# Kernel tuning notes

Measured on AMD Instinct MI355X. Metric: run time of the kernel, lower is better.

Reference implementation:

```python
import jax, jax.numpy as jnp
import numpy as np
import math

D_MODEL = 1024
N_HEADS = 16
D_HEAD = D_MODEL // N_HEADS
DECAY_MAX = 0.99  # buggy torch init: only the LAST head's decay rate survives the loop
LN_EPS = 1e-5


def setup_inputs() -> dict:
    key = jax.random.key(0)
    ks = jax.random.split(key, 12)
    B, S = 2, 2048
    x = jax.random.normal(ks[0], (B, S, D_MODEL), dtype=jnp.float32)
    def w(k):
        return jax.random.normal(k, (D_MODEL, D_MODEL), dtype=jnp.float32) * 0.02
    return {
        "x": x,
        "Wq": w(ks[1]), "bq": jnp.zeros((D_MODEL,), jnp.float32),
        "Wk": w(ks[2]), "bk": jnp.zeros((D_MODEL,), jnp.float32),
        "Wv": w(ks[3]), "bv": jnp.zeros((D_MODEL,), jnp.float32),
        "Wg": w(ks[4]), "bg": jnp.zeros((D_MODEL,), jnp.float32),
        "Wo": w(ks[5]), "bo": jnp.zeros((D_MODEL,), jnp.float32),
        "gamma": jnp.ones((D_MODEL,), jnp.float32),
        "beta": jnp.zeros((D_MODEL,), jnp.float32),
    }


def _decay_mask(S):
    # faithful to torch buffer: decay_matrix[i,j] = DECAY_MAX**(i-j) for j<=i else 0
    i = jnp.arange(S, dtype=jnp.float32)[:, None]
    j = jnp.arange(S, dtype=jnp.float32)[None, :]
    diff = i - j
    return jnp.where(diff >= 0, jnp.power(jnp.float32(DECAY_MAX), diff), 0.0)  # [S,S]


def reference(x, Wq, bq, Wk, bk, Wv, bv, Wg, bg, Wo, bo, gamma, beta):
    B, S, D = x.shape
    H, DH = N_HEADS, D_HEAD
    # projections -> [B,H,S,DH]
    Q = (x @ Wq + bq).reshape(B, S, H, DH).transpose(0, 2, 1, 3)
    K = (x @ Wk + bk).reshape(B, S, H, DH).transpose(0, 2, 1, 3)
    V = (x @ Wv + bv).reshape(B, S, H, DH).transpose(0, 2, 1, 3)
    scores = jnp.einsum('bhsd,bhtd->bhst', Q, K) / math.sqrt(DH)  # [B,H,S,S]
    mask = _decay_mask(S)  # [S,S], broadcast over B,H (head-independent per torch bug)
    retained = jnp.einsum('bhst,bhtd->bhsd', scores * mask, V)
    retained = retained.transpose(0, 2, 1, 3).reshape(B, S, D)
    # LayerNorm over last dim
    mu = jnp.mean(retained, axis=-1, keepdims=True)
    var = jnp.var(retained, axis=-1, keepdims=True)
    normed = (retained - mu) * jax.lax.rsqrt(var + LN_EPS) * gamma + beta
    G = jax.nn.sigmoid(x @ Wg + bg)
    return (normed * G) @ Wo + bo  # dropout = identity (eval)
```

## Files before the change

### kernel.cpp

```cpp
#include <hip/hip_runtime.h>

typedef __attribute__((ext_vector_type(4))) float f32x4;
typedef __attribute__((ext_vector_type(8))) short bf16x8;
typedef unsigned short USHORT;

static __device__ __forceinline__ float bf2f(USHORT u) {
    return __uint_as_float(((unsigned)u) << 16);
}
static __device__ __forceinline__ USHORT f2bf(float f) {
    unsigned u = __float_as_uint(f);
    unsigned r = u + 0x7FFF + ((u >> 16) & 1);
    return (USHORT)(r >> 16);
}

#define GLDS16(gp, lp) __builtin_amdgcn_global_load_lds(                      \
    (const __attribute__((address_space(1))) unsigned int*)(gp),              \
    (__attribute__((address_space(3))) unsigned int*)(lp), 16, 0, 0)

#define FULL_BARRIER() asm volatile("s_waitcnt vmcnt(0) lgkmcnt(0)\ns_barrier" ::: "memory")

#define D64 0.52559648f
#define L2D (-0.014499569695115089f)

struct PrepArgs { const float* src[5]; USHORT* dst[5]; const float* x; USHORT* xb; };

__global__ __launch_bounds__(256) void k_prep(PrepArgs pa) {
    const int z = blockIdx.z;
    const int tid = threadIdx.x;
    __shared__ USHORT t[64][65];
    if (z < 5) {
        const float* __restrict__ W  = pa.src[z];
        USHORT* __restrict__      WT = pa.dst[z];
        const int k0 = blockIdx.y * 64, n0 = blockIdx.x * 64;
#pragma unroll
        for (int s = 0; s < 4; s++) {
            int slot = tid + s * 256;
            int row = slot >> 4, c4 = (slot & 15) * 4;
            float4 vv = *(const float4*)&W[(size_t)(k0 + row) * 1024 + n0 + c4];
            t[row][c4 + 0] = f2bf(vv.x);
            t[row][c4 + 1] = f2bf(vv.y);
            t[row][c4 + 2] = f2bf(vv.z);
            t[row][c4 + 3] = f2bf(vv.w);
        }
        __syncthreads();
#pragma unroll
        for (int s = 0; s < 2; s++) {
            int slot = tid + s * 256;
            int n = slot >> 3, c8 = (slot & 7) * 8;
            USHORT tmp[8];
#pragma unroll
            for (int u = 0; u < 8; u++) tmp[u] = t[c8 + u][n];
            *(int4*)&WT[(size_t)(n0 + n) * 1024 + k0 + c8] = *(int4*)tmp;
        }
    } else {
        const int bi = blockIdx.y * 16 + blockIdx.x;
        const float* xs = pa.x + (size_t)bi * 16384;
        USHORT* xd = pa.xb + (size_t)bi * 16384;
#pragma unroll
        for (int u = 0; u < 16; u++) {
            int idx = u * 1024 + tid * 4;
            float4 v = *(const float4*)&xs[idx];
            *(ushort4*)&xd[idx] = make_ushort4(f2bf(v.x), f2bf(v.y), f2bf(v.z), f2bf(v.w));
        }
    }
}

struct GArgs {
    const USHORT* A;
    const USHORT* W[4];
    const float*  bias[4];
    void*         dst[4];
    USHORT*       dstv;
    float         scale[4];
    int           mode[4];
};

__global__ __launch_bounds__(256, 2) void k_gemm(GArgs ga) {
    const int z = blockIdx.z;
    const USHORT* __restrict__ A  = ga.A;
    const USHORT* __restrict__ BT = ga.W[z];
    __shared__ USHORT As[2][128 * 32];
    __shared__ USHORT Bs[2][128 * 32];
    const int tid = threadIdx.x;
    const int m0 = blockIdx.y * 128, n0 = blockIdx.x * 128;
    const int w = tid >> 6, l = tid & 63, lr = l & 15, q = l >> 4;
    const int wr = w >> 1, wc = w & 1;
    const int srow = tid >> 2, sco = (tid & 3) * 8;
    f32x4 acc[4][4] = {};
    GLDS16(&A [(size_t)(m0 + srow)      * 1024 + sco], &As[0][srow * 32 + sco]);
    GLDS16(&A [(size_t)(m0 + srow + 64) * 1024 + sco], &As[0][(srow + 64) * 32 + sco]);
    GLDS16(&BT[(size_t)(n0 + srow)      * 1024 + sco], &Bs[0][srow * 32 + sco]);
    GLDS16(&BT[(size_t)(n0 + srow + 64) * 1024 + sco], &Bs[0][(srow + 64) * 32 + sco]);
    for (int kt = 0; kt < 32; kt++) {
        const int cur = kt & 1;
        FULL_BARRIER();
        if (kt + 1 < 32) {
            const int k1 = (kt + 1) * 32;
            const int nxt = 1 - cur;
            GLDS16(&A [(size_t)(m0 + srow)      * 1024 + k1 + sco], &As[nxt][srow * 32 + sco]);
            GLDS16(&A [(size_t)(m0 + srow + 64) * 1024 + k1 + sco], &As[nxt][(srow + 64) * 32 + sco]);
            GLDS16(&BT[(size_t)(n0 + srow)      * 1024 + k1 + sco], &Bs[nxt][srow * 32 + sco]);
            GLDS16(&BT[(size_t)(n0 + srow + 64) * 1024 + k1 + sco], &Bs[nxt][(srow + 64) * 32 + sco]);
        }
        bf16x8 af[4], bfr[4];
#pragma unroll
        for (int mi = 0; mi < 4; mi++)
            af[mi] = *(const bf16x8*)&As[cur][(wr * 64 + mi * 16 + lr) * 32 + q * 8];
#pragma unroll
        for (int ni = 0; ni < 4; ni++)
            bfr[ni] = *(const bf16x8*)&Bs[cur][(wc * 64 + ni * 16 + lr) * 32 + q * 8];
#pragma unroll
        for (int mi = 0; mi < 4; mi++)
#pragma unroll
            for (int ni = 0; ni < 4; ni++)
                acc[mi][ni] = __builtin_amdgcn_mfma_f32_16x16x32_bf16(
                    af[mi], bfr[ni], acc[mi][ni], 0, 0, 0);
    }
    const float scale = ga.scale[z];
    const int mode = ga.mode[z];
    const float* __restrict__ bias = ga.bias[z];
#pragma unroll
    for (int ni = 0; ni < 4; ni++) {
        int col = n0 + wc * 64 + ni * 16 + lr;
        float bv = bias[col];
#pragma unroll
        for (int mi = 0; mi < 4; mi++) {
            int r0 = m0 + wr * 64 + mi * 16 + q * 4;
            float vr[4];
#pragma unroll
            for (int r = 0; r < 4; r++) {
                float v = acc[mi][ni][r] + bv;
                if (mode == 1) v = 1.0f / (1.0f + __expf(-v));
                vr[r] = v * scale;
            }
            if (mode == 3) {
                float* df = (float*)ga.dst[z];
#pragma unroll
                for (int r = 0; r < 4; r++)
                    df[(size_t)(r0 + r) * 1024 + col] = vr[r];
            } else if (mode == 2) {
                int b = r0 >> 11, s = r0 & 2047;
                int h = col >> 6, d = col & 63;
                const float NP1 = 1.0101010101010102f;
                float c0 = exp2f(-L2D * (float)(s & 63));
                float c1 = c0 * NP1, c2 = c1 * NP1, c3 = c2 * NP1;
                *(ushort4*)&ga.dstv[(size_t)(((b * 16 + h) * 64) + d) * 2048 + s] =
                    make_ushort4(f2bf(vr[0] * c0), f2bf(vr[1] * c1),
                                 f2bf(vr[2] * c2), f2bf(vr[3] * c3));
            } else {
                USHORT* db = (USHORT*)ga.dst[z];
#pragma unroll
                for (int r = 0; r < 4; r++)
                    db[(size_t)(r0 + r) * 1024 + col] = f2bf(vr[r]);
            }
        }
    }
}

__global__ __launch_bounds__(256) void k_attn_u(const USHORT* __restrict__ K,
                                                const USHORT* __restrict__ VT,
                                                float* __restrict__ U) {
    const int bh = blockIdx.x, c = blockIdx.y;
    const int b = bh >> 4, h = bh & 15;
    const int tid = threadIdx.x, w = tid >> 6, l = tid & 63, lr = l & 15, q = l >> 4;
    __shared__ USHORT KT[64 * 72];
    __shared__ USHORT Vs[64 * 72];
#pragma unroll
    for (int s = 0; s < 2; s++) {
        int slot = tid + s * 256;
        int row = slot >> 3, co = (slot & 7) * 8;
        USHORT kv[8];
        *(int4*)kv = *(const int4*)&K[(size_t)(b * 2048 + c * 64 + row) * 1024 + h * 64 + co];
#pragma unroll
        for (int u = 0; u < 8; u++) KT[(co + u) * 72 + row] = kv[u];
        *(int4*)&Vs[row * 72 + co] =
            *(const int4*)&VT[(size_t)(bh * 64 + row) * 2048 + c * 64 + co];
    }
    __syncthreads();
    f32x4 acc[4] = {};
    bf16x8 av[2];
#pragma unroll
    for (int kk = 0; kk < 2; kk++)
        av[kk] = *(const bf16x8*)&Vs[(w * 16 + lr) * 72 + kk * 32 + q * 8];
#pragma unroll
    for (int dkt = 0; dkt < 4; dkt++)
#pragma unroll
        for (int kk = 0; kk < 2; kk++) {
            bf16x8 bk = *(const bf16x8*)&KT[(dkt * 16 + lr) * 72 + kk * 32 + q * 8];
            acc[dkt] = __builtin_amdgcn_mfma_f32_16x16x32_bf16(av[kk], bk, acc[dkt], 0, 0, 0);
        }
    float* slot = U + (size_t)(bh * 32 + c) * 4096;
#pragma unroll
    for (int dkt = 0; dkt < 4; dkt++)
#pragma unroll
        for (int r = 0; r < 4; r++)
            slot[(w * 16 + q * 4 + r) * 64 + dkt * 16 + lr] = acc[dkt][r] * D64;
}

__global__ __launch_bounds__(256, 2) void k_apply(const USHORT* __restrict__ Q,
                                                  const USHORT* __restrict__ K,
                                                  const USHORT* __restrict__ VT,
                                                  const float* __restrict__ U,
                                                  USHORT* __restrict__ R,
                                                  float* __restrict__ stats) {
    const int bh = blockIdx.x, c = blockIdx.y;
    const int b = bh >> 4, h = bh & 15;
    const int i0 = c * 64;
    const int tid = threadIdx.x, w = tid >> 6, l = tid & 63, lr = l & 15, q = l >> 4;
    __shared__ USHORT Qs[64 * 72];
    __shared__ USHORT Ks[64 * 72];
    __shared__ USHORT Vs[64 * 72];
    __shared__ USHORT Ps[4][16 * 72];
    __shared__ unsigned Spk[4096];
#pragma unroll
    for (int s = 0; s < 2; s++) {
        int slot = tid + s * 256;
        int row = slot >> 3, c8 = (slot & 7) * 8;
        USHORT q8[8];
        *(int4*)q8 = *(const int4*)&Q[(size_t)(b * 2048 + i0 + row) * 1024 + h * 64 + c8];
        const float fr = exp2f(L2D * (float)row);
#pragma unroll
        for (int u = 0; u < 8; u++) q8[u] = f2bf(bf2f(q8[u]) * fr);
        *(int4*)&Qs[row * 72 + c8] = *(int4*)q8;
        *(int4*)&Ks[row * 72 + c8] =
            *(const int4*)&K[(size_t)(b * 2048 + i0 + row) * 1024 + h * 64 + c8];
        *(int4*)&Vs[row * 72 + c8] =
            *(const int4*)&VT[(size_t)(bh * 64 + row) * 2048 + i0 + c8];
    }
    if (c > 0) {
        float sa[16] = {};
        const float* Ub = U + (size_t)bh * 32 * 4096 + tid * 16;
        for (int cp = 0; cp < c; cp++) {
            const float* p = Ub + (size_t)cp * 4096;
#pragma unroll
            for (int u4 = 0; u4 < 4; u4++) {
                float4 uv = *(const float4*)(p + u4 * 4);
                sa[u4 * 4 + 0] = sa[u4 * 4 + 0] * D64 + uv.x;
                sa[u4 * 4 + 1] = sa[u4 * 4 + 1] * D64 + uv.y;
                sa[u4 * 4 + 2] = sa[u4 * 4 + 2] * D64 + uv.z;
                sa[u4 * 4 + 3] = sa[u4 * 4 + 3] * D64 + uv.w;
            }
        }
#pragma unroll
        for (int u = 0; u < 16; u++) {
            USHORT hi = f2bf(sa[u]);
            float  lo = sa[u] - bf2f(hi);
            Spk[tid * 16 + u] = (unsigned)hi | ((unsigned)f2bf(lo) << 16);
        }
    }
    __syncthreads();
    bf16x8 bqf[2];
#pragma unroll
    for (int kk = 0; kk < 2; kk++)
        bqf[kk] = *(const bf16x8*)&Qs[(w * 16 + lr) * 72 + kk * 32 + q * 8];
    f32x4 accr[4] = {};
    if (c > 0) {
#pragma unroll
        for (int dt = 0; dt < 4; dt++)
#pragma unroll
            for (int kk = 0; kk < 2; kk++) {
                const unsigned* sp = &Spk[(dt * 16 + lr) * 64 + kk * 32 + q * 8];
                uint4 pa = *(const uint4*)sp;
                uint4 pb = *(const uint4*)(sp + 4);
                unsigned pk[8] = { pa.x, pa.y, pa.z, pa.w, pb.x, pb.y, pb.z, pb.w };
                bf16x8 hi, lo;
#pragma unroll
                for (int u = 0; u < 8; u++) {
                    hi[u] = (short)(pk[u] & 0xffffu);
                    lo[u] = (short)(pk[u] >> 16);
                }
                accr[dt] = __builtin_amdgcn_mfma_f32_16x16x32_bf16(hi, bqf[kk], accr[dt], 0, 0, 0);
                accr[dt] = __builtin_amdgcn_mfma_f32_16x16x32_bf16(lo, bqf[kk], accr[dt], 0, 0, 0);
            }
    }
    {
        f32x4 accp[4] = {};
#pragma unroll
        for (int kk = 0; kk < 2; kk++)
#pragma unroll
            for (int jt = 0; jt < 4; jt++) {
                bf16x8 akf = *(const bf16x8*)&Ks[(jt * 16 + lr) * 72 + kk * 32 + q * 8];
                accp[jt] = __builtin_amdgcn_mfma_f32_16x16x32_bf16(akf, bqf[kk], accp[jt], 0, 0, 0);
            }
        const int ii = w * 16 + lr;
#pragma unroll
        for (int jt = 0; jt < 4; jt++) {
            const int jj = jt * 16 + q * 4;
            float v0 = (jj + 0 <= ii) ? accp[jt][0] : 0.0f;
            float v1 = (jj + 1 <= ii) ? accp[jt][1] : 0.0f;
            float v2 = (jj + 2 <= ii) ? accp[jt][2] : 0.0f;
            float v3 = (jj + 3 <= ii) ? accp[jt][3] : 0.0f;
            unsigned w0 = __builtin_amdgcn_perm(
                __float_as_uint(v1), __float_as_uint(v0), 0x07060302u);
            unsigned w1 = __builtin_amdgcn_perm(
                __float_as_uint(v3), __float_as_uint(v2), 0x07060302u);
            *(uint2*)&Ps[w][lr * 72 + jt * 16 + q * 4] = make_uint2(w0, w1);
        }
        asm volatile("s_waitcnt lgkmcnt(0)" ::: "memory");
#pragma unroll
        for (int kk = 0; kk < 2; kk++) {
            bf16x8 bpf = *(const bf16x8*)&Ps[w][lr * 72 + kk * 32 + q * 8];
#pragma unroll
            for (int dt = 0; dt < 4; dt++) {
                bf16x8 avf = *(const bf16x8*)&Vs[(dt * 16 + lr) * 72 + kk * 32 + q * 8];
                accr[dt] = __builtin_amdgcn_mfma_f32_16x16x32_bf16(avf, bpf, accr[dt], 0, 0, 0);
            }
        }
    }
    {
        float s1 = 0.f, s2 = 0.f;
#pragma unroll
        for (int dt = 0; dt < 4; dt++)
#pragma unroll
            for (int r = 0; r < 4; r++) {
                float v = accr[dt][r];
                s1 += v; s2 += v * v;
            }
        s1 += __shfl_down(s1, 32); s2 += __shfl_down(s2, 32);
        s1 += __shfl_down(s1, 16); s2 += __shfl_down(s2, 16);
        if (q == 0) {
            int row = b * 2048 + i0 + w * 16 + lr;
            *(float2*)&stats[((size_t)row * 16 + h) * 2] = make_float2(s1, s2);
        }
    }
    {
        const int i = i0 + w * 16 + lr;
#pragma unroll
        for (int dt = 0; dt < 4; dt++) {
            f32x4 a = accr[dt];
            *(ushort4*)&R[(size_t)(b * 2048 + i) * 1024 + h * 64 + dt * 16 + q * 4] =
                make_ushort4(f2bf(a[0]), f2bf(a[1]), f2bf(a[2]), f2bf(a[3]));
        }
    }
}

__global__ __launch_bounds__(256) void k_ln_gate(const USHORT* __restrict__ R,
                                                 const USHORT* __restrict__ G,
                                                 const float* __restrict__ stats,
                                                 const float* __restrict__ gamma,
                                                 const float* __restrict__ beta,
                                                 USHORT* __restrict__ NG) {
    const int row = blockIdx.x, tid = threadIdx.x;
    float s1 = 0.f, s2 = 0.f;
    const float* sp = &stats[(size_t)row * 32];
#pragma unroll
    for (int hh = 0; hh < 8; hh++) {
        float4 v = *(const float4*)(sp + hh * 4);
        s1 += v.x + v.z; s2 += v.y + v.w;
    }
    const float mu  = s1 * (1.0f / 1024.0f);
    const float var = s2 * (1.0f / 1024.0f) - mu * mu;
    const float inv = rsqrtf(fmaxf(var, 0.0f) + 1e-5f);
    ushort4 rv = *(const ushort4*)&R[(size_t)row * 1024 + tid * 4];
    ushort4 g4 = *(const ushort4*)&G[(size_t)row * 1024 + tid * 4];
    float4 gm = *(const float4*)&gamma[tid * 4];
    float4 bt = *(const float4*)&beta[tid * 4];
    float  vv[4]  = { bf2f(rv.x), bf2f(rv.y), bf2f(rv.z), bf2f(rv.w) };
    USHORT gg[4]  = { g4.x, g4.y, g4.z, g4.w };
    float  gmm[4] = { gm.x, gm.y, gm.z, gm.w };
    float  btt[4] = { bt.x, bt.y, bt.z, bt.w };
    USHORT o4[4];
#pragma unroll
    for (int u = 0; u < 4; u++) {
        float nv = (vv[u] - mu) * inv * gmm[u] + btt[u];
        o4[u] = f2bf(nv * bf2f(gg[u]));
    }
    *(ushort4*)&NG[(size_t)row * 1024 + tid * 4] = make_ushort4(o4[0], o4[1], o4[2], o4[3]);
}

extern "C" void kernel_launch(void* const* d_in, const int* in_sizes, int n_in,
                              void* d_out, int out_size, void* d_ws, size_t ws_size,
                              hipStream_t stream) {
    const float* x     = (const float*)d_in[0];
    const float* Wq    = (const float*)d_in[1];
    const float* bq    = (const float*)d_in[2];
    const float* Wk    = (const float*)d_in[3];
    const float* bk    = (const float*)d_in[4];
    const float* Wv    = (const float*)d_in[5];
    const float* bv    = (const float*)d_in[6];
    const float* Wg    = (const float*)d_in[7];
    const float* bg    = (const float*)d_in[8];
    const float* Wo    = (const float*)d_in[9];
    const float* bo    = (const float*)d_in[10];
    const float* gamma = (const float*)d_in[11];
    const float* beta  = (const float*)d_in[12];

    char* ws = (char*)d_ws;
    const size_t MB = 1 << 20;
    USHORT* WqT = (USHORT*)(ws + 0 * MB);
    USHORT* WkT = (USHORT*)(ws + 2 * MB);
    USHORT* WvT = (USHORT*)(ws + 4 * MB);
    USHORT* WgT = (USHORT*)(ws + 6 * MB);
    USHORT* WoT = (USHORT*)(ws + 8 * MB);
    USHORT* Qb  = (USHORT*)(ws + 10 * MB);
    USHORT* Kb  = (USHORT*)(ws + 18 * MB);
    USHORT* VTb = (USHORT*)(ws + 26 * MB);
    USHORT* Gb  = (USHORT*)(ws + 34 * MB);
    float*  Sts = (float*) (ws + 42 * MB);
    USHORT* NGb = Qb;
    USHORT* Xb  = (USHORT*)d_out;
    float*  Ust = (float*)d_out;

    {
        PrepArgs pa;
        pa.src[0] = Wq; pa.src[1] = Wk; pa.src[2] = Wv; pa.src[3] = Wg; pa.src[4] = Wo;
        pa.dst[0] = WqT; pa.dst[1] = WkT; pa.dst[2] = WvT; pa.dst[3] = WgT; pa.dst[4] = WoT;
        pa.x = x; pa.xb = Xb;
        k_prep<<<dim3(16, 16, 6), 256, 0, stream>>>(pa);
    }
    {
        GArgs ga;
        ga.A = Xb;
        ga.W[0] = WqT; ga.W[1] = WkT; ga.W[2] = WvT; ga.W[3] = WgT;
        ga.bias[0] = bq; ga.bias[1] = bk; ga.bias[2] = bv; ga.bias[3] = bg;
        ga.dst[0] = Qb; ga.dst[1] = Kb; ga.dst[2] = nullptr; ga.dst[3] = Gb;
        ga.dstv = VTb;
        ga.scale[0] = 0.125f; ga.scale[1] = 1.0f; ga.scale[2] = 1.0f; ga.scale[3] = 1.0f;
        ga.mode[0] = 0; ga.mode[1] = 0; ga.mode[2] = 2; ga.mode[3] = 1;
        k_gemm<<<dim3(8, 32, 4), 256, 0, stream>>>(ga);
    }
    k_attn_u<<<dim3(32, 32), 256, 0, stream>>>(Kb, VTb, Ust);
    k_apply<<<dim3(32, 32), 256, 0, stream>>>(Qb, Kb, VTb, Ust, Kb, Sts);
    k_ln_gate<<<4096, 256, 0, stream>>>(Kb, Gb, Sts, gamma, beta, NGb);
    {
        GArgs go;
        go.A = NGb;
        for (int i = 0; i < 4; i++) {
            go.W[i] = WoT; go.bias[i] = bo; go.dst[i] = d_out;
            go.scale[i] = 1.0f; go.mode[i] = 3;
        }
        go.dstv = nullptr;
        k_gemm<<<dim3(8, 32, 1), 256, 0, stream>>>(go);
    }
}
```

Before: 221.7 us.

## Add 256x256-tile 8-wave pipelined GEMM for fused QKVG projection

Adds a new projection GEMM kernel with 256x256 output tiles, 512 threads and 128KB of dynamic LDS. It uses direct global-to-LDS loads with an XOR swizzle, a double-buffered half-K pipeline, and raised wave priority around the MFMA bursts. Larger tiles raise arithmetic intensity and cut global traffic for the four fused projections. The cost is a grid of only 256 blocks, which may underfill the GPU, plus heavy register and LDS pressure. The old kernel stays as a fallback if the LDS attribute cannot be set.

```diff
diff --git a/kernel.cpp b/kernel.cpp
--- a/kernel.cpp
+++ b/kernel.cpp
@@ -157,6 +157,131 @@
     }
 }
 
+#define LDSA(buf, kh) (((buf) * 2 + (kh)) * 8192)
+#define LDSB(buf, kh) (32768 + ((buf) * 2 + (kh)) * 8192)
+#define BAR() asm volatile("s_barrier" ::: "memory")
+#define VM8() asm volatile("s_waitcnt vmcnt(8)" ::: "memory")
+
+#define STAGE_A(ks, kh, buf) do {                                             \
+    const USHORT* s_ = aBase + (ks) * 64 + (kh) * 32;                         \
+    GLDS16(s_,          &lds[LDSA(buf, kh) + ldsT]);                          \
+    GLDS16(s_ + 131072, &lds[LDSA(buf, kh) + 4096 + ldsT]); } while (0)
+
+#define STAGE_B(ks, kh, buf) do {                                             \
+    const USHORT* s_ = bBase + (ks) * 64 + (kh) * 32;                         \
+    GLDS16(s_,          &lds[LDSB(buf, kh) + ldsT]);                          \
+    GLDS16(s_ + 131072, &lds[LDSB(buf, kh) + 4096 + ldsT]); } while (0)
+
+#define PHASE256(buf, kh, mg, LOADB, STAGE_STMT, WAITSTMT) do {               \
+    _Pragma("unroll")                                                         \
+    for (int mi = 0; mi < 4; mi++)                                            \
+        af[mi] = *(const bf16x8*)&lds[LDSA(buf, kh) + aoff + ((mg) * 4 + mi) * 512]; \
+    if (LOADB) {                                                              \
+        _Pragma("unroll")                                                     \
+        for (int ni = 0; ni < 4; ni++)                                        \
+            bfrag[ni] = *(const bf16x8*)&lds[LDSB(buf, kh) + boff + ni * 512];\
+    }                                                                         \
+    STAGE_STMT;                                                               \
+    BAR();                                                                    \
+    __builtin_amdgcn_s_setprio(1);                                            \
+    _Pragma("unroll")                                                         \
+    for (int mi = 0; mi < 4; mi++)                                            \
+        _Pragma("unroll")                                                     \
+        for (int ni = 0; ni < 4; ni++)                                        \
+            acc[(mg) * 4 + mi][ni] = __builtin_amdgcn_mfma_f32_16x16x32_bf16( \
+                af[mi], bfrag[ni], acc[(mg) * 4 + mi][ni], 0, 0, 0);          \
+    __builtin_amdgcn_s_setprio(0);                                            \
+    WAITSTMT;                                                                 \
+    BAR();                                                                    \
+} while (0)
+
+__global__ __launch_bounds__(512, 2) void k_gemm256(GArgs ga) {
+    extern __shared__ USHORT lds[];
+    int bid = blockIdx.x + 4 * (blockIdx.y + 16 * blockIdx.z);
+    bid = (bid & 7) * 32 + (bid >> 3);
+    const int bz = bid >> 6;
+    const int by = (bid >> 2) & 15;
+    const int bx = bid & 3;
+    const int z = bz;
+    const USHORT* __restrict__ A  = ga.A;
+    const USHORT* __restrict__ BT = ga.W[z];
+    const int m0 = by * 256, n0 = bx * 256;
+    const int tid = threadIdx.x;
+    const int wid = tid >> 6, l = tid & 63, lr = l & 15, q = l >> 4;
+    const int wr = wid >> 2, wc = wid & 3;
+    const int srow = tid >> 2;
+    const int scol = (((tid & 3) ^ ((tid >> 2) & 3)) << 3);
+    const USHORT* aBase = A  + (size_t)(m0 + srow) * 1024 + scol;
+    const USHORT* bBase = BT + (size_t)(n0 + srow) * 1024 + scol;
+    const int ldsT = tid * 8;
+    const int kread = ((q ^ (lr & 3)) << 3);
+    const int aoff = (wr * 128 + lr) * 32 + kread;
+    const int boff = (wc * 64 + lr) * 32 + kread;
+    f32x4 acc[8][4] = {};
+    bf16x8 af[4], bfrag[4];
+
+    STAGE_A(0, 0, 0); STAGE_B(0, 0, 0);
+    STAGE_A(0, 1, 0); STAGE_B(0, 1, 0);
+    STAGE_A(1, 0, 1); STAGE_B(1, 0, 1);
+    VM8();
+    BAR();
+
+    for (int kt = 0; kt < 16; kt += 2) {
+        const int ks1 = kt + 1;
+        const int ks2 = (kt + 2 < 16) ? kt + 2 : 15;
+        const int ks3 = (kt + 2 < 16) ? kt + 2 : 15;
+        const int ks4 = (kt + 3 < 16) ? kt + 3 : 15;
+        PHASE256(0, 0, 0, 1, STAGE_A(ks1, 1, 1), (void)0);
+        PHASE256(0, 0, 1, 0, STAGE_B(ks1, 1, 1), VM8());
+        PHASE256(0, 1, 0, 1, STAGE_A(ks2, 0, 0), (void)0);
+        PHASE256(0, 1, 1, 0, STAGE_B(ks2, 0, 0), VM8());
+        PHASE256(1, 0, 0, 1, STAGE_A(ks3, 1, 0), (void)0);
+        PHASE256(1, 0, 1, 0, STAGE_B(ks3, 1, 0), VM8());
+        PHASE256(1, 1, 0, 1, STAGE_A(ks4, 0, 1), (void)0);
+        PHASE256(1, 1, 1, 0, STAGE_B(ks4, 0, 1), VM8());
+    }
+
+    const float scale = ga.scale[z];
+    const int mode = ga.mode[z];
+    const float* __restrict__ bias = ga.bias[z];
+#pragma unroll
+    for (int ni = 0; ni < 4; ni++) {
+        int col = n0 + wc * 64 + ni * 16 + lr;
+        float bv = bias[col];
+#pragma unroll
+        for (int mi = 0; mi < 8; mi++) {
+            int r0 = m0 + wr * 128 + mi * 16 + q * 4;
+            float vr[4];
+#pragma unroll
+            for (int r = 0; r < 4; r++) {
+                float v = acc[mi][ni][r] + bv;
+                if (mode == 1) v = 1.0f / (1.0f + __expf(-v));
+                vr[r] = v * scale;
+            }
+            if (mode == 3) {
+                float* df = (float*)ga.dst[z];
+#pragma unroll
+                for (int r = 0; r < 4; r++)
+                    df[(size_t)(r0 + r) * 1024 + col] = vr[r];
+            } else if (mode == 2) {
+                int b = r0 >> 11, s = r0 & 2047;
+                int h = col >> 6, d = col & 63;
+                const float NP1 = 1.0101010101010102f;
+                float c0 = exp2f(-L2D * (float)(s & 63));
+                float c1 = c0 * NP1, c2 = c1 * NP1, c3 = c2 * NP1;
+                *(ushort4*)&ga.dstv[(size_t)(((b * 16 + h) * 64) + d) * 2048 + s] =
+                    make_ushort4(f2bf(vr[0] * c0), f2bf(vr[1] * c1),
+                                 f2bf(vr[2] * c2), f2bf(vr[3] * c3));
+            } else {
+                USHORT* db = (USHORT*)ga.dst[z];
+#pragma unroll
+                for (int r = 0; r < 4; r++)
+                    db[(size_t)(r0 + r) * 1024 + col] = f2bf(vr[r]);
+            }
+        }
+    }
+}
+
 __global__ __launch_bounds__(256) void k_attn_u(const USHORT* __restrict__ K,
                                                 const USHORT* __restrict__ VT,
                                                 float* __restrict__ U) {
@@ -409,6 +534,13 @@
         k_prep<<<dim3(16, 16, 6), 256, 0, stream>>>(pa);
     }
     {
+        static int s_256ok = -1;
+        if (s_256ok < 0) {
+            hipError_t e = hipFuncSetAttribute(
+                reinterpret_cast<const void*>(&k_gemm256),
+                hipFuncAttributeMaxDynamicSharedMemorySize, 131072);
+            s_256ok = (e == hipSuccess) ? 1 : 0;
+        }
         GArgs ga;
         ga.A = Xb;
         ga.W[0] = WqT; ga.W[1] = WkT; ga.W[2] = WvT; ga.W[3] = WgT;
@@ -417,7 +549,10 @@
         ga.dstv = VTb;
         ga.scale[0] = 0.125f; ga.scale[1] = 1.0f; ga.scale[2] = 1.0f; ga.scale[3] = 1.0f;
         ga.mode[0] = 0; ga.mode[1] = 0; ga.mode[2] = 2; ga.mode[3] = 1;
-        k_gemm<<<dim3(8, 32, 4), 256, 0, stream>>>(ga);
+        if (s_256ok)
+            k_gemm256<<<dim3(4, 16, 4), 512, 131072, stream>>>(ga);
+        else
+            k_gemm<<<dim3(8, 32, 4), 256, 0, stream>>>(ga);
     }
     k_attn_u<<<dim3(32, 32), 256, 0, stream>>>(Kb, VTb, Ust);
     k_apply<<<dim3(32, 32), 256, 0, stream>>>(Qb, Kb, VTb, Ust, Kb, Sts);
```

Result: no change. 221.2 us (-0.2%).
